# Performance work log

Hardware: AMD Instinct MI355X
Metric: run time of the kernel (lower is better)

The kernel has to match this reference:

```python
import jax, jax.numpy as jnp
import numpy as np

B, N, E = 16, 4096, 65536
CIN, COUT, MAX_DEGREE = 128, 128, 3


def _spmm(rows, cols, vals, x):
    # one sample: y[r] = sum_e vals[e] * x[cols[e]] scattered to rows[e]
    return jax.ops.segment_sum(vals[:, None] * x[cols], rows, num_segments=N)

_spmm_b = jax.vmap(_spmm)  # over batch


def setup_inputs() -> dict:
    key = jax.random.key(0)
    ks = jax.random.split(key, 6)
    x = jax.random.normal(ks[0], (B, N, CIN), dtype=jnp.float32)
    vals = jax.random.normal(ks[1], (B, E), dtype=jnp.float32) * 0.1  # rescaled-Laplacian-like values
    weights = jax.random.normal(ks[2], (MAX_DEGREE + 1, CIN, COUT), dtype=jnp.float32) * 0.1
    bias = jnp.full((COUT,), 0.1, dtype=jnp.float32)
    rows = jax.random.randint(ks[3], (B, E), 0, N, dtype=jnp.int32)
    cols = jax.random.randint(ks[4], (B, E), 0, N, dtype=jnp.int32)
    return {"x": x, "vals": vals, "weights": weights, "bias": bias,
            "rows": rows, "cols": cols}


def reference(x, vals, weights, bias, rows, cols):
    # Chebyshev recursion: T0 = x, T1 = L x, Tk = 2 L T_{k-1} - T_{k-2}
    cheb0 = x
    out = jnp.einsum('bni,io->bno', cheb0, weights[0])
    cheb1 = _spmm_b(rows, cols, vals, x)
    out = out + jnp.einsum('bni,io->bno', cheb1, weights[1])
    for k in range(2, MAX_DEGREE + 1):
        cheb2 = 2.0 * _spmm_b(rows, cols, vals, cheb1) - cheb0
        out = out + jnp.einsum('bni,io->bno', cheb2, weights[k])
        cheb0, cheb1 = cheb1, cheb2
    return jax.nn.relu(out + bias)
```

## Files before the change

kernel.cpp:

```cpp
#include <hip/hip_runtime.h>
#include <hip/hip_bf16.h>
#include <stdint.h>

#define B_ 16
#define N_ 4096
#define E_ 65536
#define C_ 128
#define ECAP 81920

typedef unsigned short u16;
typedef unsigned int u32;
using f32x4 = __attribute__((ext_vector_type(4))) float;
using s16x8 = __attribute__((ext_vector_type(8))) short;

__device__ __forceinline__ u16 f2bf(float f) {
  u32 u = __builtin_bit_cast(u32, f);
  u = (u + 0x7FFFu + ((u >> 16) & 1u)) >> 16;
  return (u16)u;
}
__device__ __forceinline__ float bflo(u32 u) {
  return __builtin_bit_cast(float, u << 16);
}
__device__ __forceinline__ float bfhi(u32 u) {
  return __builtin_bit_cast(float, u & 0xFFFF0000u);
}


__global__ __launch_bounds__(256) void prep_kernel(const float* __restrict__ x,
                                                   u16* __restrict__ xb,
                                                   const float* __restrict__ w,
                                                   u16* __restrict__ wf,
                                                   const int* __restrict__ rows,
                                                   int* __restrict__ hist) {
  int blk = blockIdx.x;
  int t = threadIdx.x;
  if (blk < 4096) {
    int xcd = blk & 7;
    int j   = blk >> 3;
    int b   = xcd * 2 + (j >> 8);
    size_t base = (size_t)b * N_ * C_ + ((j & 255) * 256 + t) * 8;
    const float4* xp = reinterpret_cast<const float4*>(x + base);
    float4 a0 = xp[0];
    float4 a1 = xp[1];
    uint4 p;
    p.x = (u32)f2bf(a0.x) | ((u32)f2bf(a0.y) << 16);
    p.y = (u32)f2bf(a0.z) | ((u32)f2bf(a0.w) << 16);
    p.z = (u32)f2bf(a1.x) | ((u32)f2bf(a1.y) << 16);
    p.w = (u32)f2bf(a1.z) | ((u32)f2bf(a1.w) << 16);
    *reinterpret_cast<uint4*>(xb + base) = p;
  } else if (blk < 4352) {
    int tid = (blk - 4096) * 256 + t;
    int j  = tid & 7;
    int l  = (tid >> 3) & 63;
    int ct = (tid >> 9) & 7;
    int ks = tid >> 12;
    int g  = l >> 4;
    int k  = ks * 32 + g * 8 + j;
    int kk = k >> 7;
    int i  = k & 127;
    int o  = ct * 16 + (l & 15);
    float a = w[(kk * C_ + i) * C_ + o];
    float r;
    if (kk == 0)      r = a - w[(2 * C_ + i) * C_ + o];
    else if (kk == 1) r = a - 3.f * w[(3 * C_ + i) * C_ + o];
    else if (kk == 2) r = 2.f * a;
    else              r = 4.f * a;
    wf[tid] = f2bf(r);
  } else {
    __shared__ int h[N_];
    int hblk = blk - 4352;
    int b = hblk >> 4;
    int c = hblk & 15;
    #pragma unroll
    for (int i = 0; i < 16; ++i) h[t + 256 * i] = 0;
    __syncthreads();
    int ebase = b * E_ + c * 4096;
    #pragma unroll
    for (int i = 0; i < 16; ++i) {
      int r = rows[ebase + t + 256 * i];
      atomicAdd(&h[r], 1);
    }
    __syncthreads();
    int4* hg = reinterpret_cast<int4*>(hist + (size_t)hblk * 4096);
    const int4* hl = reinterpret_cast<const int4*>(h);
    #pragma unroll
    for (int i = 0; i < 4; ++i) hg[t + 256 * i] = hl[t + 256 * i];
  }
}

__global__ __launch_bounds__(256) void rowscan_kernel(int* __restrict__ hist,
                                                      int* __restrict__ cnt) {
  int rg = blockIdx.x * 256 + threadIdx.x;
  int b = rg >> 12;
  int r = rg & 4095;
  int base = (b * 16) * 4096 + r;
  int h[16];
  #pragma unroll
  for (int c = 0; c < 16; ++c) h[c] = hist[base + c * 4096];
  int run = 0;
  #pragma unroll
  for (int c = 0; c < 16; ++c) {
    int v = h[c];
    hist[base + c * 4096] = run;
    run += v;
  }
  cnt[rg] = run;
}

__global__ __launch_bounds__(256) void scatter2_kernel(const int* __restrict__ rows,
                                                       const int* __restrict__ cols,
                                                       const float* __restrict__ vals,
                                                       const int* __restrict__ cnt,
                                                       const int* __restrict__ hist,
                                                       u32* __restrict__ ecv,
                                                       int* __restrict__ off) {
  __shared__ int base[N_];
  __shared__ int cur[N_];
  __shared__ int offl[N_];
  __shared__ int psum[256];
  int xcd = blockIdx.x & 7;
  int j   = blockIdx.x >> 3;
  int b   = xcd * 2 + (j >> 4);
  int c   = j & 15;
  int t   = threadIdx.x;
  int local[16];
  int s = 0;
  int cbase = b * N_ + t * 16;
  #pragma unroll
  for (int i = 0; i < 16; ++i) {
    local[i] = (cnt[cbase + i] + 3) & ~3;
    s += local[i];
  }
  psum[t] = s;
  __syncthreads();
  if (t == 0) {
    int run = 0;
    for (int i = 0; i < 256; ++i) { int v = psum[i]; psum[i] = run; run += v; }
  }
  __syncthreads();
  {
    int run = psum[t];
    #pragma unroll
    for (int i = 0; i < 16; ++i) { offl[t * 16 + i] = run; run += local[i]; }
    if (c == 0) {
      #pragma unroll
      for (int i = 0; i < 16; ++i) off[b * (N_ + 1) + t * 16 + i] = offl[t * 16 + i];
      if (t == 255) off[b * (N_ + 1) + N_] = run;
    }
  }
  __syncthreads();
  const int* hb = hist + (b * 16 + c) * 4096;
  #pragma unroll
  for (int i = 0; i < 16; ++i) {
    int idx = t + 256 * i;
    base[idx] = offl[idx] + hb[idx];
    cur[idx] = 0;
  }
  __syncthreads();
  int ebase = b * E_ + c * 4096;
  u32* ecvb = ecv + (size_t)b * ECAP;
  #pragma unroll
  for (int i = 0; i < 16; ++i) {
    int e = ebase + t + 256 * i;
    int r = rows[e];
    int rank = atomicAdd(&cur[r], 1);
    u32 pv = (u32)cols[e] | ((u32)f2bf(vals[e]) << 16);
    ecvb[base[r] + rank] = pv;
  }
  if (c == 0) {
    #pragma unroll
    for (int i = 0; i < 16; ++i) {
      int r = t + 256 * i;
      int real = cnt[b * N_ + r];
      int pbase = offl[r] + real;
      int pad = (-real) & 3;
      for (int k = 0; k < pad; ++k) ecvb[pbase + k] = 0;
    }
  }
}


__global__ __launch_bounds__(256) void spmm_kernel(const u16* __restrict__ src,
                                                   u16* __restrict__ dst,
                                                   const u32* __restrict__ ecv,
                                                   const int* __restrict__ off) {
  int lane = threadIdx.x & 63;
  int wv   = threadIdx.x >> 6;
  int xcd  = blockIdx.x & 7;
  int j    = blockIdx.x >> 3;
  int b    = xcd * 2 + (j >> 9);
  int rp   = ((j & 511) << 2) | wv;
  int eg   = lane >> 4;
  int cl   = lane & 15;
  int n    = rp * 2 + (eg >> 1);
  int sub  = eg & 1;
  int s4 = off[b * (N_ + 1) + n] >> 2;
  int e4 = off[b * (N_ + 1) + n + 1] >> 2;
  const uint4* ecv4 = reinterpret_cast<const uint4*>(ecv + (size_t)b * ECAP);
  const u16* srcb = src + (size_t)b * N_ * C_;
  float acc[8];
  #pragma unroll
  for (int t = 0; t < 8; ++t) acc[t] = 0.f;
  for (int gp = s4 + sub; gp < e4; gp += 2) {
    uint4 cv = ecv4[gp];
    u32 e0 = cv.x, e1 = cv.y, e2 = cv.z, e3 = cv.w;
    uint4 u0 = *reinterpret_cast<const uint4*>(srcb + (size_t)(e0 & 0xFFFFu) * C_ + cl * 8);
    uint4 u1 = *reinterpret_cast<const uint4*>(srcb + (size_t)(e1 & 0xFFFFu) * C_ + cl * 8);
    uint4 u2 = *reinterpret_cast<const uint4*>(srcb + (size_t)(e2 & 0xFFFFu) * C_ + cl * 8);
    uint4 u3 = *reinterpret_cast<const uint4*>(srcb + (size_t)(e3 & 0xFFFFu) * C_ + cl * 8);
    float v0 = bfhi(e0), v1 = bfhi(e1), v2 = bfhi(e2), v3 = bfhi(e3);
    acc[0] = fmaf(v0, bflo(u0.x), acc[0]);
    acc[1] = fmaf(v0, bfhi(u0.x), acc[1]);
    acc[2] = fmaf(v0, bflo(u0.y), acc[2]);
    acc[3] = fmaf(v0, bfhi(u0.y), acc[3]);
    acc[4] = fmaf(v0, bflo(u0.z), acc[4]);
    acc[5] = fmaf(v0, bfhi(u0.z), acc[5]);
    acc[6] = fmaf(v0, bflo(u0.w), acc[6]);
    acc[7] = fmaf(v0, bfhi(u0.w), acc[7]);
    acc[0] = fmaf(v1, bflo(u1.x), acc[0]);
    acc[1] = fmaf(v1, bfhi(u1.x), acc[1]);
    acc[2] = fmaf(v1, bflo(u1.y), acc[2]);
    acc[3] = fmaf(v1, bfhi(u1.y), acc[3]);
    acc[4] = fmaf(v1, bflo(u1.z), acc[4]);
    acc[5] = fmaf(v1, bfhi(u1.z), acc[5]);
    acc[6] = fmaf(v1, bflo(u1.w), acc[6]);
    acc[7] = fmaf(v1, bfhi(u1.w), acc[7]);
    acc[0] = fmaf(v2, bflo(u2.x), acc[0]);
    acc[1] = fmaf(v2, bfhi(u2.x), acc[1]);
    acc[2] = fmaf(v2, bflo(u2.y), acc[2]);
    acc[3] = fmaf(v2, bfhi(u2.y), acc[3]);
    acc[4] = fmaf(v2, bflo(u2.z), acc[4]);
    acc[5] = fmaf(v2, bfhi(u2.z), acc[5]);
    acc[6] = fmaf(v2, bflo(u2.w), acc[6]);
    acc[7] = fmaf(v2, bfhi(u2.w), acc[7]);
    acc[0] = fmaf(v3, bflo(u3.x), acc[0]);
    acc[1] = fmaf(v3, bfhi(u3.x), acc[1]);
    acc[2] = fmaf(v3, bflo(u3.y), acc[2]);
    acc[3] = fmaf(v3, bfhi(u3.y), acc[3]);
    acc[4] = fmaf(v3, bflo(u3.z), acc[4]);
    acc[5] = fmaf(v3, bfhi(u3.z), acc[5]);
    acc[6] = fmaf(v3, bflo(u3.w), acc[6]);
    acc[7] = fmaf(v3, bfhi(u3.w), acc[7]);
  }
  #pragma unroll
  for (int t = 0; t < 8; ++t) acc[t] += __shfl_xor(acc[t], 16);
  if (sub == 0) {
    size_t ro = ((size_t)(b * N_ + n)) * C_ + cl * 8;
    uint4 p;
    p.x = (u32)f2bf(acc[0]) | ((u32)f2bf(acc[1]) << 16);
    p.y = (u32)f2bf(acc[2]) | ((u32)f2bf(acc[3]) << 16);
    p.z = (u32)f2bf(acc[4]) | ((u32)f2bf(acc[5]) << 16);
    p.w = (u32)f2bf(acc[6]) | ((u32)f2bf(acc[7]) << 16);
    *reinterpret_cast<uint4*>(dst + ro) = p;
  }
}


__global__ __launch_bounds__(512) void gemm_kernel(const u16* __restrict__ xb,
                                                   const u16* __restrict__ g1,
                                                   const u16* __restrict__ g2,
                                                   const u16* __restrict__ g3,
                                                   const u16* __restrict__ wf,
                                                   const float* __restrict__ bias,
                                                   float* __restrict__ out) {
  __shared__ u16 wls[65536];
  int tid = threadIdx.x;
  #pragma unroll
  for (int i = 0; i < 16; ++i) {
    int chunk = i * 512 + tid;
    reinterpret_cast<uint4*>(wls)[chunk] = reinterpret_cast<const uint4*>(wf)[chunk];
  }
  __syncthreads();
  int lane = tid & 63;
  int w = tid >> 6;
  int xcd = blockIdx.x & 7;
  int j = blockIdx.x >> 3;
  int b = xcd * 2 + (j >> 4);
  int mb = b * N_ + (j & 15) * 256 + w * 32;
  int g  = lane >> 4;
  int rl = lane & 15;
  const u16* srcs[4] = {xb, g1, g2, g3};
  f32x4 acc0[8], acc1[8];
  #pragma unroll
  for (int t = 0; t < 8; ++t) {
    acc0[t] = (f32x4){0.f, 0.f, 0.f, 0.f};
    acc1[t] = (f32x4){0.f, 0.f, 0.f, 0.f};
  }
  size_t mrow = (size_t)(mb + rl) * C_;
  for (int ks = 0; ks < 16; ++ks) {
    const u16* ap = srcs[ks >> 2] + mrow + (ks & 3) * 32 + g * 8;
    s16x8 a0 = *reinterpret_cast<const s16x8*>(ap);
    s16x8 a1 = *reinterpret_cast<const s16x8*>(ap + 16 * C_);
    const u16* wp = wls + (ks * 8) * 512 + lane * 8;
    #pragma unroll
    for (int ct = 0; ct < 8; ++ct) {
      s16x8 bfv = *reinterpret_cast<const s16x8*>(wp + ct * 512);
      acc0[ct] = __builtin_amdgcn_mfma_f32_16x16x32_bf16(a0, bfv, acc0[ct], 0, 0, 0);
      acc1[ct] = __builtin_amdgcn_mfma_f32_16x16x32_bf16(a1, bfv, acc1[ct], 0, 0, 0);
    }
  }
  #pragma unroll
  for (int ct = 0; ct < 8; ++ct) {
    int o = ct * 16 + rl;
    float bo = bias[o];
    #pragma unroll
    for (int r = 0; r < 4; ++r) {
      int m0 = mb + g * 4 + r;
      int m1 = mb + 16 + g * 4 + r;
      float v0 = acc0[ct][r] + bo;
      float v1 = acc1[ct][r] + bo;
      out[(size_t)m0 * C_ + o] = v0 > 0.f ? v0 : 0.f;
      out[(size_t)m1 * C_ + o] = v1 > 0.f ? v1 : 0.f;
    }
  }
}


extern "C" void kernel_launch(void* const* d_in, const int* in_sizes, int n_in,
                              void* d_out, int out_size, void* d_ws, size_t ws_size,
                              hipStream_t stream) {
  (void)in_sizes; (void)n_in; (void)out_size; (void)ws_size;
  const float* x    = (const float*)d_in[0];
  const float* vals = (const float*)d_in[1];
  const float* wts  = (const float*)d_in[2];
  const float* bias = (const float*)d_in[3];
  const int*   rows = (const int*)d_in[4];
  const int*   cols = (const int*)d_in[5];
  float* out = (float*)d_out;

  const size_t SB = (size_t)B_ * N_ * C_ * sizeof(u16);
  char* ws = (char*)d_ws;
  u16* xb = (u16*)ws;
  u16* g1 = (u16*)(ws + SB);
  u16* g2 = (u16*)(ws + 2 * SB);
  u16* g3 = (u16*)(ws + 3 * SB);
  char* meta = ws + 4 * SB;
  int* hist = (int*)meta;
  u32* ecv  = (u32*)(meta + 4194304);
  int* cnt  = (int*)(meta + 9437184);
  int* off  = (int*)(meta + 9699328);
  u16* wf   = (u16*)(meta + 9961536);

  prep_kernel<<<4608, 256, 0, stream>>>(x, xb, wts, wf, rows, hist);
  rowscan_kernel<<<256, 256, 0, stream>>>(hist, cnt);
  scatter2_kernel<<<256, 256, 0, stream>>>(rows, cols, vals, cnt, hist, ecv, off);
  spmm_kernel<<<8192, 256, 0, stream>>>(xb, g1, ecv, off);
  spmm_kernel<<<8192, 256, 0, stream>>>(g1, g2, ecv, off);
  spmm_kernel<<<8192, 256, 0, stream>>>(g2, g3, ecv, off);
  gemm_kernel<<<256, 512, 0, stream>>>(xb, g1, g2, g3, wf, bias, out);
}
```

Measured before the change: 116.5 us.

## Store higher-order Chebyshev terms in FP8 to halve SpMM gather traffic

The first SpMM now also writes an FP8 copy of its output into the output buffer, used as scratch. A new SpMM kernel gathers FP8 rows (16 channels per lane, 8 edge slots per wave) to produce the second and third Chebyshev terms directly in FP8. The GEMM converts those FP8 operands back to bf16 before the MFMA. This halves the bytes moved in the gather-heavy SpMM passes and the GEMM reads, at the cost of much lower precision (e4m3 without scaling) and extra convert instructions, which risks failing accuracy tolerance.

Measured after the change: 147.5 us. 26.5% more time.

```diff
diff --git a/kernel.cpp b/kernel.cpp
--- a/kernel.cpp
+++ b/kernel.cpp
@@ -10,7 +10,9 @@
 
 typedef unsigned short u16;
 typedef unsigned int u32;
+typedef unsigned char u8;
 using f32x4 = __attribute__((ext_vector_type(4))) float;
+using f32x2 = __attribute__((ext_vector_type(2))) float;
 using s16x8 = __attribute__((ext_vector_type(8))) short;
 
 __device__ __forceinline__ u16 f2bf(float f) {
@@ -182,6 +184,7 @@
 
 __global__ __launch_bounds__(256) void spmm_kernel(const u16* __restrict__ src,
                                                    u16* __restrict__ dst,
+                                                   u8* __restrict__ dst8,
                                                    const u32* __restrict__ ecv,
                                                    const int* __restrict__ off) {
   int lane = threadIdx.x & 63;
@@ -252,14 +255,92 @@
     p.z = (u32)f2bf(acc[4]) | ((u32)f2bf(acc[5]) << 16);
     p.w = (u32)f2bf(acc[6]) | ((u32)f2bf(acc[7]) << 16);
     *reinterpret_cast<uint4*>(dst + ro) = p;
+    int q0 = 0, q1 = 0;
+    q0 = __builtin_amdgcn_cvt_pk_fp8_f32(acc[0], acc[1], q0, false);
+    q0 = __builtin_amdgcn_cvt_pk_fp8_f32(acc[2], acc[3], q0, true);
+    q1 = __builtin_amdgcn_cvt_pk_fp8_f32(acc[4], acc[5], q1, false);
+    q1 = __builtin_amdgcn_cvt_pk_fp8_f32(acc[6], acc[7], q1, true);
+    *reinterpret_cast<uint2*>(dst8 + ro) = make_uint2((u32)q0, (u32)q1);
+  }
+}
+
+
+__global__ __launch_bounds__(256) void spmm8_kernel(const u8* __restrict__ src8,
+                                                    u8* __restrict__ dst8,
+                                                    const u32* __restrict__ ecv,
+                                                    const int* __restrict__ off) {
+  int lane = threadIdx.x & 63;
+  int wv   = threadIdx.x >> 6;
+  int xcd  = blockIdx.x & 7;
+  int j    = blockIdx.x >> 3;
+  int b    = xcd * 2 + (j >> 10);
+  int n    = ((j & 1023) << 2) | wv;
+  int slot = lane >> 3;
+  int cl   = lane & 7;
+  int s4 = off[b * (N_ + 1) + n] >> 2;
+  int e4 = off[b * (N_ + 1) + n + 1] >> 2;
+  const uint4* ecv4 = reinterpret_cast<const uint4*>(ecv + (size_t)b * ECAP);
+  const u8* srcb = src8 + (size_t)b * N_ * C_;
+  float acc[16];
+  #pragma unroll
+  for (int t = 0; t < 16; ++t) acc[t] = 0.f;
+  int comp = slot & 3;
+  for (int g = s4 + (slot >> 2); g < e4; g += 2) {
+    uint4 cv = ecv4[g];
+    u32 ew = comp == 0 ? cv.x : comp == 1 ? cv.y : comp == 2 ? cv.z : cv.w;
+    float v = bfhi(ew);
+    uint4 q = *reinterpret_cast<const uint4*>(srcb + (size_t)(ew & 0xFFFFu) * C_ + cl * 16);
+    f32x2 p0 = __builtin_amdgcn_cvt_pk_f32_fp8((int)q.x, false);
+    f32x2 p1 = __builtin_amdgcn_cvt_pk_f32_fp8((int)q.x, true);
+    f32x2 p2 = __builtin_amdgcn_cvt_pk_f32_fp8((int)q.y, false);
+    f32x2 p3 = __builtin_amdgcn_cvt_pk_f32_fp8((int)q.y, true);
+    f32x2 p4 = __builtin_amdgcn_cvt_pk_f32_fp8((int)q.z, false);
+    f32x2 p5 = __builtin_amdgcn_cvt_pk_f32_fp8((int)q.z, true);
+    f32x2 p6 = __builtin_amdgcn_cvt_pk_f32_fp8((int)q.w, false);
+    f32x2 p7 = __builtin_amdgcn_cvt_pk_f32_fp8((int)q.w, true);
+    acc[0]  = fmaf(v, p0.x, acc[0]);
+    acc[1]  = fmaf(v, p0.y, acc[1]);
+    acc[2]  = fmaf(v, p1.x, acc[2]);
+    acc[3]  = fmaf(v, p1.y, acc[3]);
+    acc[4]  = fmaf(v, p2.x, acc[4]);
+    acc[5]  = fmaf(v, p2.y, acc[5]);
+    acc[6]  = fmaf(v, p3.x, acc[6]);
+    acc[7]  = fmaf(v, p3.y, acc[7]);
+    acc[8]  = fmaf(v, p4.x, acc[8]);
+    acc[9]  = fmaf(v, p4.y, acc[9]);
+    acc[10] = fmaf(v, p5.x, acc[10]);
+    acc[11] = fmaf(v, p5.y, acc[11]);
+    acc[12] = fmaf(v, p6.x, acc[12]);
+    acc[13] = fmaf(v, p6.y, acc[13]);
+    acc[14] = fmaf(v, p7.x, acc[14]);
+    acc[15] = fmaf(v, p7.y, acc[15]);
+  }
+  #pragma unroll
+  for (int t = 0; t < 16; ++t) {
+    acc[t] += __shfl_xor(acc[t], 8);
+    acc[t] += __shfl_xor(acc[t], 16);
+    acc[t] += __shfl_xor(acc[t], 32);
+  }
+  if (slot == 0) {
+    size_t ro = ((size_t)(b * N_ + n)) * C_ + cl * 16;
+    int q0 = 0, q1 = 0, q2 = 0, q3 = 0;
+    q0 = __builtin_amdgcn_cvt_pk_fp8_f32(acc[0],  acc[1],  q0, false);
+    q0 = __builtin_amdgcn_cvt_pk_fp8_f32(acc[2],  acc[3],  q0, true);
+    q1 = __builtin_amdgcn_cvt_pk_fp8_f32(acc[4],  acc[5],  q1, false);
+    q1 = __builtin_amdgcn_cvt_pk_fp8_f32(acc[6],  acc[7],  q1, true);
+    q2 = __builtin_amdgcn_cvt_pk_fp8_f32(acc[8],  acc[9],  q2, false);
+    q2 = __builtin_amdgcn_cvt_pk_fp8_f32(acc[10], acc[11], q2, true);
+    q3 = __builtin_amdgcn_cvt_pk_fp8_f32(acc[12], acc[13], q3, false);
+    q3 = __builtin_amdgcn_cvt_pk_fp8_f32(acc[14], acc[15], q3, true);
+    *reinterpret_cast<uint4*>(dst8 + ro) = make_uint4((u32)q0, (u32)q1, (u32)q2, (u32)q3);
   }
 }
 
 
 __global__ __launch_bounds__(512) void gemm_kernel(const u16* __restrict__ xb,
                                                    const u16* __restrict__ g1,
-                                                   const u16* __restrict__ g2,
-                                                   const u16* __restrict__ g3,
+                                                   const u8* __restrict__ g2_8,
+                                                   const u8* __restrict__ g3_8,
                                                    const u16* __restrict__ wf,
                                                    const float* __restrict__ bias,
                                                    float* __restrict__ out) {
@@ -279,7 +360,6 @@
   int mb = b * N_ + (j & 15) * 256 + w * 32;
   int g  = lane >> 4;
   int rl = lane & 15;
-  const u16* srcs[4] = {xb, g1, g2, g3};
   f32x4 acc0[8], acc1[8];
   #pragma unroll
   for (int t = 0; t < 8; ++t) {
@@ -287,10 +367,35 @@
     acc1[t] = (f32x4){0.f, 0.f, 0.f, 0.f};
   }
   size_t mrow = (size_t)(mb + rl) * C_;
+  #pragma unroll
   for (int ks = 0; ks < 16; ++ks) {
-    const u16* ap = srcs[ks >> 2] + mrow + (ks & 3) * 32 + g * 8;
-    s16x8 a0 = *reinterpret_cast<const s16x8*>(ap);
-    s16x8 a1 = *reinterpret_cast<const s16x8*>(ap + 16 * C_);
+    s16x8 a0, a1;
+    const int sel = ks >> 2;
+    if (sel < 2) {
+      const u16* ap = (sel == 0 ? xb : g1) + mrow + (ks & 3) * 32 + g * 8;
+      a0 = *reinterpret_cast<const s16x8*>(ap);
+      a1 = *reinterpret_cast<const s16x8*>(ap + 16 * C_);
+    } else {
+      const u8* ap8 = (sel == 2 ? g2_8 : g3_8) + mrow + (ks & 3) * 32 + g * 8;
+      uint2 q0 = *reinterpret_cast<const uint2*>(ap8);
+      uint2 q1 = *reinterpret_cast<const uint2*>(ap8 + 16 * C_);
+      f32x2 p0 = __builtin_amdgcn_cvt_pk_f32_fp8((int)q0.x, false);
+      f32x2 p1 = __builtin_amdgcn_cvt_pk_f32_fp8((int)q0.x, true);
+      f32x2 p2 = __builtin_amdgcn_cvt_pk_f32_fp8((int)q0.y, false);
+      f32x2 p3 = __builtin_amdgcn_cvt_pk_f32_fp8((int)q0.y, true);
+      a0[0] = (short)f2bf(p0.x); a0[1] = (short)f2bf(p0.y);
+      a0[2] = (short)f2bf(p1.x); a0[3] = (short)f2bf(p1.y);
+      a0[4] = (short)f2bf(p2.x); a0[5] = (short)f2bf(p2.y);
+      a0[6] = (short)f2bf(p3.x); a0[7] = (short)f2bf(p3.y);
+      f32x2 r0 = __builtin_amdgcn_cvt_pk_f32_fp8((int)q1.x, false);
+      f32x2 r1 = __builtin_amdgcn_cvt_pk_f32_fp8((int)q1.x, true);
+      f32x2 r2 = __builtin_amdgcn_cvt_pk_f32_fp8((int)q1.y, false);
+      f32x2 r3 = __builtin_amdgcn_cvt_pk_f32_fp8((int)q1.y, true);
+      a1[0] = (short)f2bf(r0.x); a1[1] = (short)f2bf(r0.y);
+      a1[2] = (short)f2bf(r1.x); a1[3] = (short)f2bf(r1.y);
+      a1[4] = (short)f2bf(r2.x); a1[5] = (short)f2bf(r2.y);
+      a1[6] = (short)f2bf(r3.x); a1[7] = (short)f2bf(r3.y);
+    }
     const u16* wp = wls + (ks * 8) * 512 + lane * 8;
     #pragma unroll
     for (int ct = 0; ct < 8; ++ct) {
@@ -332,20 +437,21 @@
   char* ws = (char*)d_ws;
   u16* xb = (u16*)ws;
   u16* g1 = (u16*)(ws + SB);
-  u16* g2 = (u16*)(ws + 2 * SB);
-  u16* g3 = (u16*)(ws + 3 * SB);
+  u8* g2_8 = (u8*)(ws + 2 * SB);
+  u8* g3_8 = (u8*)(ws + 2 * SB + SB / 2);
   char* meta = ws + 4 * SB;
   int* hist = (int*)meta;
   u32* ecv  = (u32*)(meta + 4194304);
   int* cnt  = (int*)(meta + 9437184);
   int* off  = (int*)(meta + 9699328);
   u16* wf   = (u16*)(meta + 9961536);
+  u8* g1_8 = (u8*)d_out;
 
   prep_kernel<<<4608, 256, 0, stream>>>(x, xb, wts, wf, rows, hist);
   rowscan_kernel<<<256, 256, 0, stream>>>(hist, cnt);
   scatter2_kernel<<<256, 256, 0, stream>>>(rows, cols, vals, cnt, hist, ecv, off);
-  spmm_kernel<<<8192, 256, 0, stream>>>(xb, g1, ecv, off);
-  spmm_kernel<<<8192, 256, 0, stream>>>(g1, g2, ecv, off);
-  spmm_kernel<<<8192, 256, 0, stream>>>(g2, g3, ecv, off);
-  gemm_kernel<<<256, 512, 0, stream>>>(xb, g1, g2, g3, wf, bias, out);
-}
+  spmm_kernel<<<8192, 256, 0, stream>>>(xb, g1, g1_8, ecv, off);
+  spmm8_kernel<<<16384, 256, 0, stream>>>(g1_8, g2_8, ecv, off);
+  spmm8_kernel<<<16384, 256, 0, stream>>>(g2_8, g3_8, ecv, off);
+  gemm_kernel<<<256, 512, 0, stream>>>(xb, g1, g2_8, g3_8, wf, bias, out);
+}
```
